# Kernel optimization log

Measured on AMD Instinct MI355X. Metric: run time of the kernel, lower is better.

Reference implementation:

```python
import jax, jax.numpy as jnp
import numpy as np

B, S, HID = 2, 2048, 2048
H, KV, D = 32, 4, 128
G = H // KV
EPS = 1e-6
SCALE = D ** -0.5
ROPE_THETA = 1000000.0


def setup_inputs() -> dict:
    key = jax.random.key(0)
    ks = jax.random.split(key, 6)
    hidden_states = jax.random.normal(ks[0], (B, S, HID), jnp.float32)
    # real RoPE tables (position_embeddings passed into forward)
    inv_freq = 1.0 / (ROPE_THETA ** (np.arange(0, D, 2, dtype=np.float32) / D))
    ang = np.arange(S, dtype=np.float32)[:, None] * inv_freq[None, :]  # [S, D/2]
    emb = np.concatenate([ang, ang], axis=-1)  # [S, D]
    cos = jnp.broadcast_to(jnp.asarray(np.cos(emb)), (B, S, D))
    sin = jnp.broadcast_to(jnp.asarray(np.sin(emb)), (B, S, D))
    sd = 0.02
    wq = jax.random.normal(ks[1], (H * D, HID), jnp.float32) * sd
    wk = jax.random.normal(ks[2], (KV * D, HID), jnp.float32) * sd
    wv = jax.random.normal(ks[3], (KV * D, HID), jnp.float32) * sd
    wo = jax.random.normal(ks[4], (HID, H * D), jnp.float32) * sd
    q_norm_w = jnp.ones((D,), jnp.float32)
    k_norm_w = jnp.ones((D,), jnp.float32)
    return {"hidden_states": hidden_states, "cos": cos, "sin": sin,
            "wq": wq, "wk": wk, "wv": wv, "wo": wo,
            "q_norm_w": q_norm_w, "k_norm_w": k_norm_w}


def _rms_norm(x, w):
    var = jnp.mean(jnp.square(x), axis=-1, keepdims=True)
    return x * jax.lax.rsqrt(var + EPS) * w


def _rotate_half(x):
    x1, x2 = jnp.split(x, 2, axis=-1)
    return jnp.concatenate([-x2, x1], axis=-1)


def _rope(x, cos, sin):
    # x: [B,S,N,D]; cos/sin: [B,S,1,D] (unsqueeze_dim=2)
    return x * cos + _rotate_half(x) * sin


def reference(hidden_states, cos, sin, wq, wk, wv, wo, q_norm_w, k_norm_w):
    x = hidden_states
    q = jnp.einsum('bsh,oh->bso', x, wq).reshape(B, S, H, D)
    k = jnp.einsum('bsh,oh->bso', x, wk).reshape(B, S, KV, D)
    v = jnp.einsum('bsh,oh->bso', x, wv).reshape(B, S, KV, D)
    q = _rms_norm(q, q_norm_w)
    k = _rms_norm(k, k_norm_w)
    c = cos[:, :, None, :]
    s = sin[:, :, None, :]
    q = _rope(q, c, s)
    k = _rope(k, c, s)
    # GQA causal attention, BSND layout
    qg = q.reshape(B, S, KV, G, D)
    scores = jnp.einsum('bqkgd,bskd->bkgqs', qg, k) * SCALE  # [B,KV,G,Sq,Sk]
    causal = jnp.tril(jnp.ones((S, S), bool))
    scores = jnp.where(causal, scores, jnp.finfo(scores.dtype).min)
    p = jax.nn.softmax(scores, axis=-1)
    out = jnp.einsum('bkgqs,bskd->bqkgd', p, v).reshape(B, S, H * D)
    return jnp.einsum('bso,ho->bsh', out, wo)
```

## Files before the change

kernel.cpp:

```cpp
#include <hip/hip_runtime.h>
#include <hip/hip_bf16.h>

typedef __attribute__((ext_vector_type(8))) short short8;
typedef __attribute__((ext_vector_type(4))) float f32x4;

#define DEVI static __device__ __forceinline__

constexpr int Bb = 2, Ss = 2048, Hh = 32, KVc = 4, Dc = 128;
constexpr float EPSc = 1e-6f;
constexpr float SCALEc = 0.08838834764831845f;

DEVI float bf2f(short s) {
  unsigned u = ((unsigned)(unsigned short)s) << 16;
  float f; __builtin_memcpy(&f, &u, 4); return f;
}
DEVI short f2bf(float f) {
  __hip_bfloat16 h = __float2bfloat16(f);
  unsigned short u; __builtin_memcpy(&u, &h, 2); return (short)u;
}

#define GLDS(gsrc, ldst) __builtin_amdgcn_global_load_lds( \
    (const __attribute__((address_space(1))) void*)(gsrc), \
    (__attribute__((address_space(3))) void*)(ldst), 16, 0, 0)

struct Cvt5 { const float* src[5]; short* dst[5]; };
__global__ void cvt_all(Cvt5 a) {
  constexpr int CUM[6] = {0, 2097152, 4194304, 4456448, 4718592, 6815744};
  const int stride = gridDim.x * blockDim.x;
  for (int i = blockIdx.x * blockDim.x + threadIdx.x; i < 6815744; i += stride) {
    int s = 0;
#pragma unroll
    for (int t = 1; t < 5; ++t) if (i >= CUM[t]) s = t;
    int j = i - CUM[s];
    float4 v = ((const float4*)a.src[s])[j];
    short4 o;
    o.x = f2bf(v.x); o.y = f2bf(v.y); o.z = f2bf(v.z); o.w = f2bf(v.w);
    ((short4*)a.dst[s])[j] = o;
  }
}

template<int MODE>
__launch_bounds__(256, 4)
__global__ void gemm_bt(const short* __restrict__ A,
                        const short* __restrict__ B0,
                        const short* __restrict__ B1,
                        const short* __restrict__ B2,
                        short* __restrict__ oq,
                        short* __restrict__ ok,
                        short* __restrict__ ov,
                        float* __restrict__ of,
                        const float* __restrict__ cosb,
                        const float* __restrict__ sinb,
                        const float* __restrict__ qnw,
                        const float* __restrict__ knw,
                        int K)
{
  __shared__ short lA[2][128 * 32];
  __shared__ short lB[2][128 * 32];
  const int tid = threadIdx.x;
  const int lane = tid & 63;
  const int wvi = tid >> 6;
  const int l15 = lane & 15, g = lane >> 4;
  const int m0 = blockIdx.x * 128;
  const int nt = blockIdx.y;
  const short* Bp; int n0, region;
  if (MODE == 0) {
    if (nt < 32)      { Bp = B0; n0 = nt * 128;        region = 0; }
    else if (nt < 36) { Bp = B1; n0 = (nt - 32) * 128; region = 1; }
    else              { Bp = B2; n0 = (nt - 36) * 128; region = 2; }
  } else { Bp = B0; n0 = nt * 128; region = 3; }

  const int wrow = wvi * 32;
  const int srow = tid >> 2, schunk = tid & 3;

  f32x4 acc[2][8] = {};

  auto STAGE = [&](int ks, int bufi) {
    const int k0 = ks * 32;
#pragma unroll
    for (int c = 0; c < 2; ++c) {
      int row = c * 64 + srow;
      int gc = schunk ^ ((row >> 1) & 3);
      GLDS(A  + (size_t)(m0 + row) * K + k0 + gc * 8, &lA[bufi][(c * 256 + tid) * 8]);
      GLDS(Bp + (size_t)(n0 + row) * K + k0 + gc * 8, &lB[bufi][(c * 256 + tid) * 8]);
    }
  };

  const int nks = K >> 5;
  STAGE(0, 0);
  STAGE(1, 1);

  for (int ks = 0; ks < nks; ++ks) {
    const int cb = ks & 1;
    if (ks + 1 < nks) asm volatile("s_waitcnt vmcnt(4)" ::: "memory");
    else              asm volatile("s_waitcnt vmcnt(0)" ::: "memory");
    __builtin_amdgcn_s_barrier();
    asm volatile("" ::: "memory");

    short8 afr[2], bfr[8];
#pragma unroll
    for (int i = 0; i < 2; ++i) {
      int ra = wrow + i * 16 + l15;
      afr[i] = *(const short8*)(&lA[cb][0] + ra * 32 + ((g ^ ((ra >> 1) & 3)) * 8));
    }
#pragma unroll
    for (int i = 0; i < 8; ++i) {
      int rb = i * 16 + l15;
      bfr[i] = *(const short8*)(&lB[cb][0] + rb * 32 + ((g ^ ((rb >> 1) & 3)) * 8));
    }
#pragma unroll
    for (int mi = 0; mi < 2; ++mi)
#pragma unroll
      for (int ni = 0; ni < 8; ++ni)
        acc[mi][ni] = __builtin_amdgcn_mfma_f32_16x16x32_bf16(afr[mi], bfr[ni], acc[mi][ni], 0, 0, 0);

    asm volatile("" ::: "memory");
    __builtin_amdgcn_s_barrier();
    if (ks + 2 < nks) STAGE(ks + 2, cb);
  }

  if (MODE == 1) {
#pragma unroll
    for (int mi = 0; mi < 2; ++mi)
#pragma unroll
      for (int r = 0; r < 4; ++r) {
        int m = m0 + wrow + mi * 16 + g * 4 + r;
#pragma unroll
        for (int ni = 0; ni < 8; ++ni)
          of[(size_t)m * 2048 + n0 + ni * 16 + l15] = acc[mi][ni][r];
      }
  } else if (region == 2) {
#pragma unroll
    for (int mi = 0; mi < 2; ++mi)
#pragma unroll
      for (int r = 0; r < 4; ++r) {
        int m = m0 + wrow + mi * 16 + g * 4 + r;
        int b = m >> 11, s = m & 2047;
#pragma unroll
        for (int ni = 0; ni < 8; ++ni) {
          int n = n0 + ni * 16 + l15;
          int kvi = n >> 7, d = n & 127;
          ov[(((size_t)b * KVc + kvi) * 128 + d) * Ss + s] = f2bf(acc[mi][ni][r]);
        }
      }
  } else {
    const float* wnorm = (region == 0) ? qnw : knw;
    float w8[8];
#pragma unroll
    for (int ni = 0; ni < 8; ++ni) w8[ni] = wnorm[ni * 16 + l15];
#pragma unroll
    for (int mi = 0; mi < 2; ++mi)
#pragma unroll
      for (int r = 0; r < 4; ++r) {
        int m = m0 + wrow + mi * 16 + g * 4 + r;
        int b = m >> 11, s = m & 2047;
        float xv[8];
        float ssq = 0.f;
#pragma unroll
        for (int ni = 0; ni < 8; ++ni) { xv[ni] = acc[mi][ni][r]; ssq += xv[ni] * xv[ni]; }
        ssq += __shfl_xor(ssq, 1);
        ssq += __shfl_xor(ssq, 2);
        ssq += __shfl_xor(ssq, 4);
        ssq += __shfl_xor(ssq, 8);
        float inv = rsqrtf(ssq * (1.0f / 128.0f) + EPSc);
        float xn[8];
#pragma unroll
        for (int ni = 0; ni < 8; ++ni) xn[ni] = xv[ni] * inv * w8[ni];
        const float* cpr = cosb + ((size_t)b * Ss + s) * Dc;
        const float* spr = sinb + ((size_t)b * Ss + s) * Dc;
#pragma unroll
        for (int ni = 0; ni < 8; ++ni) {
          int dl = ni * 16 + l15;
          float c = cpr[dl], sn = spr[dl];
          float rot = (ni < 4) ? -xn[ni + 4] : xn[ni - 4];
          float o = xn[ni] * c + rot * sn;
          int n = n0 + dl;
          if (region == 0) {
            oq[(size_t)m * 4096 + n] = f2bf(o * SCALEc);
          } else {
            int kvi = n >> 7, d = n & 127;
            ok[(((size_t)b * KVc + kvi) * Ss + s) * 128 + d] = f2bf(o);
          }
        }
      }
  }
}

__launch_bounds__(256, 2)
__global__ void attn_fwd(const short* __restrict__ qb,
                         const short* __restrict__ kbuf,
                         const short* __restrict__ vtbuf,
                         short* __restrict__ ob)
{
  __shared__ short lK[2][64 * 128];
  __shared__ short lV[2][128 * 64];
  __shared__ short lP[4][32 * 32];
  const int tid = threadIdx.x, lane = tid & 63, wvi = tid >> 6;
  const int l15 = lane & 15, g = lane >> 4;
  const int pi = blockIdx.x, h = blockIdx.y, b = blockIdx.z;
  const int kv = h >> 3;
  const short* kp = kbuf  + ((size_t)b * KVc + kv) * Ss * 128;
  const short* vp = vtbuf + ((size_t)b * KVc + kv) * 128 * Ss;
  const int krow = tid >> 4, kch = tid & 15;
  const int vrow = tid >> 3, vch = tid & 7;

  for (int which = 0; which < 2; ++which) {
    const int qt = which ? (15 - pi) : pi;
    const int qwb = qt * 128 + wvi * 32;
    const int nkt = 2 * qt + 2;

    short8 qf[2][4];
#pragma unroll
    for (int qs = 0; qs < 2; ++qs)
#pragma unroll
      for (int dc = 0; dc < 4; ++dc)
        qf[qs][dc] = *(const short8*)(qb + (size_t)(b * Ss + qwb + qs * 16 + l15) * 4096
                                         + h * 128 + dc * 32 + g * 8);

    f32x4 oacc[2][8] = {};
    float mrun[2] = { -__builtin_inff(), -__builtin_inff() };
    float lrun[2] = { 0.f, 0.f };

    auto STAGE = [&](int kt, int bufi) {
      const int kb0 = kt * 64;
#pragma unroll
      for (int c = 0; c < 4; ++c) {
        int r = c * 16 + krow;
        int gc = kch ^ (r & 7);
        GLDS(kp + (size_t)(kb0 + r) * 128 + gc * 8, &lK[bufi][(c * 256 + tid) * 8]);
      }
#pragma unroll
      for (int c = 0; c < 4; ++c) {
        int r = c * 32 + vrow;
        int gc = vch ^ (r & 7);
        GLDS(vp + (size_t)r * Ss + kb0 + gc * 8, &lV[bufi][(c * 256 + tid) * 8]);
      }
    };

    STAGE(0, 0);
    STAGE(1, 1);

    for (int kt = 0; kt < nkt; ++kt) {
      const int cb = kt & 1;
      if (kt + 1 < nkt) asm volatile("s_waitcnt vmcnt(8)" ::: "memory");
      else              asm volatile("s_waitcnt vmcnt(0)" ::: "memory");
      __builtin_amdgcn_s_barrier();
      asm volatile("" ::: "memory");

#pragma unroll
      for (int half = 0; half < 2; ++half) {
        const int kb0 = kt * 64 + half * 32;
        if (kb0 <= qwb + 31) {
          short8 kf[2][4];
#pragma unroll
          for (int ks = 0; ks < 2; ++ks)
#pragma unroll
            for (int dc = 0; dc < 4; ++dc) {
              int row = half * 32 + ks * 16 + l15;
              kf[ks][dc] = *(const short8*)(&lK[cb][0] + row * 128 + (((dc * 4 + g) ^ (row & 7)) * 8));
            }
          f32x4 st[2][2] = {};
          __builtin_amdgcn_s_setprio(1);
#pragma unroll
          for (int qs = 0; qs < 2; ++qs)
#pragma unroll
            for (int ks = 0; ks < 2; ++ks)
#pragma unroll
              for (int dc = 0; dc < 4; ++dc)
                st[qs][ks] = __builtin_amdgcn_mfma_f32_16x16x32_bf16(kf[ks][dc], qf[qs][dc], st[qs][ks], 0, 0, 0);
          __builtin_amdgcn_s_setprio(0);

          const bool need_mask = (kb0 + 31 > qwb);
#pragma unroll
          for (int qs = 0; qs < 2; ++qs) {
            const int qg = qwb + qs * 16 + l15;
            float p[8];
            float tmax = -__builtin_inff();
#pragma unroll
            for (int ks = 0; ks < 2; ++ks)
#pragma unroll
              for (int r = 0; r < 4; ++r) {
                float v = st[qs][ks][r];
                if (need_mask && (kb0 + ks * 16 + g * 4 + r > qg)) v = -__builtin_inff();
                p[ks * 4 + r] = v;
                tmax = fmaxf(tmax, v);
              }
            tmax = fmaxf(tmax, __shfl_xor(tmax, 16));
            tmax = fmaxf(tmax, __shfl_xor(tmax, 32));
            float m_use = mrun[qs];
            if (__any(tmax > m_use + 8.0f)) {
              float mnew = fmaxf(m_use, tmax);
              float scl = __expf(m_use - mnew);
              lrun[qs] *= scl;
              mrun[qs] = mnew;
#pragma unroll
              for (int r = 0; r < 4; ++r) {
                float sc = __shfl(scl, g * 4 + r);
#pragma unroll
                for (int dt = 0; dt < 8; ++dt)
                  oacc[qs][dt][r] *= sc;
              }
              m_use = mnew;
            }
            float rsum = 0.f;
#pragma unroll
            for (int j = 0; j < 8; ++j) { p[j] = __expf(p[j] - m_use); rsum += p[j]; }
            rsum += __shfl_xor(rsum, 16);
            rsum += __shfl_xor(rsum, 32);
            lrun[qs] += rsum;
            {
              int row = qs * 16 + l15;
              int sw = (row >> 1) & 3;
              short* pr = lP[wvi] + row * 32;
#pragma unroll
              for (int ks = 0; ks < 2; ++ks) {
                int idx = (((2 * ks + (g >> 1)) ^ sw) * 8) + (g & 1) * 4;
                short4 pw;
                pw.x = f2bf(p[ks * 4 + 0]);
                pw.y = f2bf(p[ks * 4 + 1]);
                pw.z = f2bf(p[ks * 4 + 2]);
                pw.w = f2bf(p[ks * 4 + 3]);
                *(short4*)(pr + idx) = pw;
              }
            }
          }
          asm volatile("" ::: "memory");
          short8 vf[8];
#pragma unroll
          for (int dt = 0; dt < 8; ++dt) {
            int row = dt * 16 + l15;
            vf[dt] = *(const short8*)(&lV[cb][0] + row * 64 + (((half * 4 + g) ^ (row & 7)) * 8));
          }
          __builtin_amdgcn_s_setprio(1);
#pragma unroll
          for (int qs = 0; qs < 2; ++qs) {
            int row = qs * 16 + l15;
            short8 pf = *(const short8*)(lP[wvi] + row * 32 + ((g ^ ((row >> 1) & 3)) * 8));
#pragma unroll
            for (int dt = 0; dt < 8; ++dt)
              oacc[qs][dt] = __builtin_amdgcn_mfma_f32_16x16x32_bf16(pf, vf[dt], oacc[qs][dt], 0, 0, 0);
          }
          __builtin_amdgcn_s_setprio(0);
          asm volatile("" ::: "memory");
        }
      }

      asm volatile("" ::: "memory");
      __builtin_amdgcn_s_barrier();
      if (kt + 2 < nkt) STAGE(kt + 2, cb);
    }

#pragma unroll
    for (int qs = 0; qs < 2; ++qs)
#pragma unroll
      for (int r = 0; r < 4; ++r) {
        float inv = 1.0f / __shfl(lrun[qs], g * 4 + r);
        int qrow = qwb + qs * 16 + g * 4 + r;
        short* op = ob + (size_t)(b * Ss + qrow) * 4096 + h * 128;
#pragma unroll
        for (int dt = 0; dt < 8; ++dt)
          op[dt * 16 + l15] = f2bf(oacc[qs][dt][r] * inv);
      }
  }
}

extern "C" void kernel_launch(void* const* d_in, const int* in_sizes, int n_in,
                              void* d_out, int out_size, void* d_ws, size_t ws_size,
                              hipStream_t stream) {
  const float* x    = (const float*)d_in[0];
  const float* cosb = (const float*)d_in[1];
  const float* sinb = (const float*)d_in[2];
  const float* wq   = (const float*)d_in[3];
  const float* wk   = (const float*)d_in[4];
  const float* wv   = (const float*)d_in[5];
  const float* wo   = (const float*)d_in[6];
  const float* qw   = (const float*)d_in[7];
  const float* kw   = (const float*)d_in[8];

  size_t off = 0;
  auto alloc = [&](size_t bytes) {
    char* p = (char*)d_ws + off;
    off += (bytes + 255) & ~(size_t)255;
    return p;
  };
  short* x_bf  = (short*)alloc((size_t)8388608 * 2);
  short* wq_bf = (short*)alloc((size_t)8388608 * 2);
  short* wk_bf = (short*)alloc((size_t)1048576 * 2);
  short* wv_bf = (short*)alloc((size_t)1048576 * 2);
  short* wo_bf = (short*)alloc((size_t)8388608 * 2);
  short* q_bf  = (short*)alloc((size_t)16777216 * 2);
  short* k_bf  = (short*)alloc((size_t)2097152 * 2);
  short* v_bf  = (short*)alloc((size_t)2097152 * 2);
  short* ao_bf = (short*)alloc((size_t)16777216 * 2);

  Cvt5 ca;
  ca.src[0] = x;    ca.dst[0] = x_bf;
  ca.src[1] = wq;   ca.dst[1] = wq_bf;
  ca.src[2] = wk;   ca.dst[2] = wk_bf;
  ca.src[3] = wv;   ca.dst[3] = wv_bf;
  ca.src[4] = wo;   ca.dst[4] = wo_bf;
  cvt_all<<<2048, 256, 0, stream>>>(ca);

  gemm_bt<0><<<dim3(32, 40), 256, 0, stream>>>(x_bf, wq_bf, wk_bf, wv_bf,
                                               q_bf, k_bf, v_bf, nullptr,
                                               cosb, sinb, qw, kw, 2048);
  attn_fwd<<<dim3(8, 32, 2), 256, 0, stream>>>(q_bf, k_bf, v_bf, ao_bf);
  gemm_bt<1><<<dim3(32, 16), 256, 0, stream>>>(ao_bf, wo_bf, nullptr, nullptr,
                                               nullptr, nullptr, nullptr, (float*)d_out,
                                               nullptr, nullptr, nullptr, nullptr, 4096);
}
```

Measured before the change: 353.4 us.

## Split Q projection into a 256x256-tile 8-wave pipelined GEMM kernel

Moves the Q projection out of the combined QKV GEMM into a dedicated kernel that uses 256x256 output tiles, 512 threads, a 64-wide K step, and a phased ping-pong LDS schedule. Each phase interleaves the next tile's loads with MFMAs and raises wave priority around the math. The fused RMSNorm/RoPE epilogue is kept. K/V projection and the output projection stay on the old 128-tile kernel. The goal is more data reuse and better load/compute overlap for the largest GEMM, at the cost of an extra launch and a large LDS and register footprint that limits occupancy.

```diff
diff --git a/kernel.cpp b/kernel.cpp
--- a/kernel.cpp
+++ b/kernel.cpp
@@ -39,21 +39,154 @@
   }
 }
 
+__launch_bounds__(512, 2)
+__global__ void gemm8q(const short* __restrict__ A,
+                       const short* __restrict__ Bp,
+                       short* __restrict__ oq,
+                       const float* __restrict__ cosb,
+                       const float* __restrict__ sinb,
+                       const float* __restrict__ qnw,
+                       int K)
+{
+  __shared__ short lA[2][256 * 64];
+  __shared__ short lB[2][256 * 64];
+
+  const int tid = threadIdx.x, lane = tid & 63;
+  const int wvi = tid >> 6;
+  const int l15 = lane & 15, g = lane >> 4;
+  const int wm = wvi >> 1, wn = wvi & 1;
+  const int m0 = blockIdx.x * 256;
+  const int n0 = blockIdx.y * 256;
+
+  f32x4 acc[4][8] = {};
+
+  auto stA = [&](int half, int slot, int kt) {
+#pragma unroll
+    for (int j = 0; j < 2; ++j) {
+      int rr = j * 64 + (tid >> 3);
+      int grow = ((rr >> 5) << 6) + half * 32 + (rr & 31);
+      GLDS(A + (size_t)(m0 + grow) * K + kt * 64 + (((tid & 7) ^ (rr & 7)) << 3),
+           &lA[slot][(half * 128 + j * 64) * 64 + tid * 8]);
+    }
+  };
+  auto stB = [&](int half, int slot, int kt) {
+#pragma unroll
+    for (int j = 0; j < 2; ++j) {
+      int rr = j * 64 + (tid >> 3);
+      int gn = ((rr >> 6) << 7) + half * 64 + (rr & 63);
+      GLDS(Bp + (size_t)(n0 + gn) * K + kt * 64 + (((tid & 7) ^ (rr & 7)) << 3),
+           &lB[slot][(half * 128 + j * 64) * 64 + tid * 8]);
+    }
+  };
+
+#define PH(SLOT, MH, NH, STG, GT) do {                                          \
+    short8 afr[2][2], bfr[4][2];                                                \
+    _Pragma("unroll")                                                           \
+    for (int mi2 = 0; mi2 < 2; ++mi2) {                                         \
+      int rp = (MH) * 128 + wm * 32 + mi2 * 16 + l15;                           \
+      _Pragma("unroll")                                                         \
+      for (int kk = 0; kk < 2; ++kk)                                            \
+        afr[mi2][kk] = *(const short8*)(&lA[SLOT][rp * 64 +                     \
+                         (((kk * 4 + g) ^ (rp & 7)) << 3)]);                    \
+    }                                                                           \
+    _Pragma("unroll")                                                           \
+    for (int nj = 0; nj < 4; ++nj) {                                            \
+      int rp = (NH) * 128 + wn * 64 + nj * 16 + l15;                            \
+      _Pragma("unroll")                                                         \
+      for (int kk = 0; kk < 2; ++kk)                                            \
+        bfr[nj][kk] = *(const short8*)(&lB[SLOT][rp * 64 +                      \
+                         (((kk * 4 + g) ^ (rp & 7)) << 3)]);                    \
+    }                                                                           \
+    STG;                                                                        \
+    asm volatile("" ::: "memory");                                              \
+    __builtin_amdgcn_s_barrier();                                               \
+    __builtin_amdgcn_s_setprio(1);                                              \
+    _Pragma("unroll")                                                           \
+    for (int mi2 = 0; mi2 < 2; ++mi2)                                           \
+      _Pragma("unroll")                                                         \
+      for (int nj = 0; nj < 4; ++nj)                                            \
+        _Pragma("unroll")                                                       \
+        for (int kk = 0; kk < 2; ++kk)                                          \
+          acc[(MH)*2 + mi2][(NH)*4 + nj] =                                      \
+            __builtin_amdgcn_mfma_f32_16x16x32_bf16(afr[mi2][kk], bfr[nj][kk],  \
+                acc[(MH)*2 + mi2][(NH)*4 + nj], 0, 0, 0);                       \
+    __builtin_amdgcn_s_setprio(0);                                              \
+    GT;                                                                         \
+    asm volatile("" ::: "memory");                                              \
+    __builtin_amdgcn_s_barrier();                                               \
+  } while (0)
+
+  const int nit = K >> 7;
+
+  stA(0, 0, 0); stB(0, 0, 0); stA(1, 0, 0); stB(1, 0, 0);
+  stA(0, 1, 1); stB(0, 1, 1);
+  asm volatile("s_waitcnt vmcnt(4)" ::: "memory");
+  __builtin_amdgcn_s_barrier();
+
+  for (int it = 0; it < nit; ++it) {
+    const int kt1 = 2 * it + 1;
+    const int k2 = 2 * it + 2, k3 = 2 * it + 3;
+    const bool pre = (it + 1 < nit);
+    PH(0, 0, 0, { stA(1, 1, kt1); }, {});
+    PH(0, 0, 1, { stB(1, 1, kt1); }, {});
+    PH(0, 1, 0, { if (pre) stA(0, 0, k2); }, {});
+    PH(0, 1, 1, { if (pre) stB(0, 0, k2); },
+               { if (pre) asm volatile("s_waitcnt vmcnt(4)" ::: "memory");
+                 else     asm volatile("s_waitcnt vmcnt(0)" ::: "memory"); });
+    PH(1, 0, 0, { if (pre) stA(1, 0, k2); }, {});
+    PH(1, 0, 1, { if (pre) stB(1, 0, k2); }, {});
+    PH(1, 1, 0, { if (pre) stA(0, 1, k3); }, {});
+    PH(1, 1, 1, { if (pre) stB(0, 1, k3); },
+               { if (pre) asm volatile("s_waitcnt vmcnt(4)" ::: "memory"); });
+  }
+#undef PH
+
+  float w8[8];
+#pragma unroll
+  for (int ni = 0; ni < 8; ++ni) w8[ni] = qnw[ni * 16 + l15];
+#pragma unroll
+  for (int mi = 0; mi < 4; ++mi)
+#pragma unroll
+    for (int r = 0; r < 4; ++r) {
+      int m = m0 + wm * 64 + mi * 16 + g * 4 + r;
+      int b = m >> 11, s = m & 2047;
+      float xv[8];
+      float ssq = 0.f;
+#pragma unroll
+      for (int ni = 0; ni < 8; ++ni) { xv[ni] = acc[mi][ni][r]; ssq += xv[ni] * xv[ni]; }
+      ssq += __shfl_xor(ssq, 1);
+      ssq += __shfl_xor(ssq, 2);
+      ssq += __shfl_xor(ssq, 4);
+      ssq += __shfl_xor(ssq, 8);
+      float inv = rsqrtf(ssq * (1.0f / 128.0f) + EPSc);
+      float xn[8];
+#pragma unroll
+      for (int ni = 0; ni < 8; ++ni) xn[ni] = xv[ni] * inv * w8[ni];
+      const float* cpr = cosb + ((size_t)b * Ss + s) * Dc;
+      const float* spr = sinb + ((size_t)b * Ss + s) * Dc;
+#pragma unroll
+      for (int ni = 0; ni < 8; ++ni) {
+        int d = ni * 16 + l15;
+        float c = cpr[d], sn = spr[d];
+        float rot = (ni < 4) ? -xn[ni + 4] : xn[ni - 4];
+        float o = xn[ni] * c + rot * sn;
+        oq[(size_t)m * 4096 + n0 + wn * 128 + d] = f2bf(o * SCALEc);
+      }
+    }
+}
+
 template<int MODE>
 __launch_bounds__(256, 4)
-__global__ void gemm_bt(const short* __restrict__ A,
-                        const short* __restrict__ B0,
-                        const short* __restrict__ B1,
-                        const short* __restrict__ B2,
-                        short* __restrict__ oq,
-                        short* __restrict__ ok,
-                        short* __restrict__ ov,
-                        float* __restrict__ of,
-                        const float* __restrict__ cosb,
-                        const float* __restrict__ sinb,
-                        const float* __restrict__ qnw,
-                        const float* __restrict__ knw,
-                        int K)
+__global__ void gemm2(const short* __restrict__ A,
+                      const short* __restrict__ B1,
+                      const short* __restrict__ B2,
+                      short* __restrict__ ok,
+                      short* __restrict__ ov,
+                      float* __restrict__ of,
+                      const float* __restrict__ cosb,
+                      const float* __restrict__ sinb,
+                      const float* __restrict__ knw,
+                      int K)
 {
   __shared__ short lA[2][128 * 32];
   __shared__ short lB[2][128 * 32];
@@ -65,10 +198,9 @@
   const int nt = blockIdx.y;
   const short* Bp; int n0, region;
   if (MODE == 0) {
-    if (nt < 32)      { Bp = B0; n0 = nt * 128;        region = 0; }
-    else if (nt < 36) { Bp = B1; n0 = (nt - 32) * 128; region = 1; }
-    else              { Bp = B2; n0 = (nt - 36) * 128; region = 2; }
-  } else { Bp = B0; n0 = nt * 128; region = 3; }
+    if (nt < 4) { Bp = B1; n0 = nt * 128;       region = 1; }
+    else        { Bp = B2; n0 = (nt - 4) * 128; region = 2; }
+  } else { Bp = B1; n0 = nt * 128; region = 3; }
 
   const int wrow = wvi * 32;
   const int srow = tid >> 2, schunk = tid & 3;
@@ -144,10 +276,9 @@
         }
       }
   } else {
-    const float* wnorm = (region == 0) ? qnw : knw;
     float w8[8];
 #pragma unroll
-    for (int ni = 0; ni < 8; ++ni) w8[ni] = wnorm[ni * 16 + l15];
+    for (int ni = 0; ni < 8; ++ni) w8[ni] = knw[ni * 16 + l15];
 #pragma unroll
     for (int mi = 0; mi < 2; ++mi)
 #pragma unroll
@@ -175,12 +306,8 @@
           float rot = (ni < 4) ? -xn[ni + 4] : xn[ni - 4];
           float o = xn[ni] * c + rot * sn;
           int n = n0 + dl;
-          if (region == 0) {
-            oq[(size_t)m * 4096 + n] = f2bf(o * SCALEc);
-          } else {
-            int kvi = n >> 7, d = n & 127;
-            ok[(((size_t)b * KVc + kvi) * Ss + s) * 128 + d] = f2bf(o);
-          }
+          int kvi = n >> 7, d = n & 127;
+          ok[(((size_t)b * KVc + kvi) * Ss + s) * 128 + d] = f2bf(o);
         }
       }
   }
@@ -401,11 +528,10 @@
   ca.src[4] = wo;   ca.dst[4] = wo_bf;
   cvt_all<<<2048, 256, 0, stream>>>(ca);
 
-  gemm_bt<0><<<dim3(32, 40), 256, 0, stream>>>(x_bf, wq_bf, wk_bf, wv_bf,
-                                               q_bf, k_bf, v_bf, nullptr,
-                                               cosb, sinb, qw, kw, 2048);
+  gemm8q<<<dim3(16, 16), 512, 0, stream>>>(x_bf, wq_bf, q_bf, cosb, sinb, qw, 2048);
+  gemm2<0><<<dim3(32, 8), 256, 0, stream>>>(x_bf, wk_bf, wv_bf, k_bf, v_bf, nullptr,
+                                            cosb, sinb, kw, 2048);
   attn_fwd<<<dim3(8, 32, 2), 256, 0, stream>>>(q_bf, k_bf, v_bf, ao_bf);
-  gemm_bt<1><<<dim3(32, 16), 256, 0, stream>>>(ao_bf, wo_bf, nullptr, nullptr,
-                                               nullptr, nullptr, nullptr, (float*)d_out,
-                                               nullptr, nullptr, nullptr, nullptr, 4096);
-}
+  gemm2<1><<<dim3(32, 16), 256, 0, stream>>>(ao_bf, wo_bf, nullptr, nullptr, nullptr,
+                                             (float*)d_out, nullptr, nullptr, nullptr, 4096);
+}
```

New measurement: 346.4 us. -2.0%, faster.
